# Kernel tuning notes

Hardware: AMD Instinct MI355X
Metric: run time of the kernel (lower is better)

The kernel has to match this reference:

```python
import jax, jax.numpy as jnp
import numpy as np

MARGIN = 0.05
TEMP = 14.0
LAM = 9.0      # opt.lambda_softmax
EPS = 1e-8
B, R, W, D, NCLS = 128, 36, 32, 256, 10


def setup_inputs() -> dict:
    key = jax.random.key(0)
    ks = jax.random.split(key, 7)
    im = jax.random.normal(ks[0], (B, R, D), jnp.float32)
    s = jax.random.normal(ks[1], (B, W, D), jnp.float32)
    s_l = jax.random.randint(ks[2], (B,), W // 2, W + 1)          # caption lengths in [16, 32]
    reg_l = jax.random.randint(ks[3], (B,), R // 2, R + 1)        # valid region counts
    im_mask = (jnp.arange(R)[None, :] < reg_l[:, None]).astype(jnp.float32)
    query_id = jax.random.randint(ks[4], (B,), 0, B)
    class_scores = jax.random.normal(ks[5], (B, NCLS), jnp.float32)
    class_labels = jax.random.randint(ks[6], (B,), 0, NCLS)
    return dict(im=im, s=s, s_l=s_l, im_mask=im_mask, query_id=query_id,
                class_scores=class_scores, class_labels=class_labels)


def _xattn_scores(im, s, s_l, im_mask):
    """Vectorized xattn_score_t2i. im:(B,R,D) images, s:(C,W,D) captions.
    Returns scores (n_image, n_caption). Zeroing pad words reproduces the
    original per-caption truncation (pad words contribute 0 to the word-dim
    l2 norm and are excluded from the final mean)."""
    wmask = (jnp.arange(W)[None, :] < s_l[:, None]).astype(s.dtype)   # (C,W)
    cap = s * wmask[:, :, None]                                        # (C,W,D)
    # attn[c,b,r,w] = <images[b,r], cap[c,w]>  (bmm in func_attention)
    attn = jnp.einsum('brd,cwd->cbrw', im, cap)
    attn = jax.nn.leaky_relu(attn, 0.1)
    # masked l2norm over the word dim (dim=2 in torch), mask over regions
    m = im_mask[None, :, :, None]                                      # (1,B,R,1)
    X = attn + (1.0 - m)
    nrm = jnp.sqrt(jnp.sum(X * X, axis=3, keepdims=True)) + EPS
    attn = (X / nrm) * m                                               # (C,B,R,W)
    # masked softmax over regions, per (caption, word); smooth = LAM
    x = jnp.swapaxes(attn, 2, 3) * LAM                                 # (C,B,W,R)
    mx = jnp.max(x, axis=3, keepdims=True)                             # unmasked max, as in source
    y = jnp.exp(x - mx) * im_mask[None, :, None, :]
    y = y / jnp.sum(y, axis=3, keepdims=True)
    # weightedContext[c,b,w,d] = sum_r images[b,r,d] * y[c,b,w,r]
    wctx = jnp.einsum('brd,cbwr->cbwd', im, y)
    # cosine similarity over d, then mean over the n_word valid words
    w12 = jnp.einsum('cwd,cbwd->cbw', cap, wctx)
    n1 = jnp.linalg.norm(cap, axis=2)                                  # (C,W)
    n2 = jnp.linalg.norm(wctx, axis=3)                                 # (C,B,W)
    cos = w12 / jnp.maximum(n1[:, None, :] * n2, EPS)
    row = jnp.sum(cos * wmask[:, None, :], axis=2) / s_l[:, None].astype(cos.dtype)
    return row.T                                                       # (n_image, n_caption)


def _contrastive_loss(im, s, s_l, im_mask, query_id):
    scores = _xattn_scores(im, s, s_l, im_mask)
    n = scores.shape[0]
    # label[i] = -100 (ignored) if query_id[i] appeared at some j < i, else i
    eq = query_id[:, None] == query_id[None, :]
    dup = jnp.any(jnp.tril(eq, k=-1), axis=1)
    labels = jnp.where(dup, -100, jnp.arange(n))
    logits = (scores - jnp.eye(n, dtype=scores.dtype) * MARGIN) * TEMP
    logZ = jax.nn.logsumexp(logits, axis=1)
    picked = jnp.take_along_axis(logits, jnp.maximum(labels, 0)[:, None], axis=1)[:, 0]
    valid = (labels >= 0).astype(scores.dtype)
    return jnp.sum((logZ - picked) * valid) / jnp.maximum(jnp.sum(valid), 1.0)


def reference(im, s, s_l, im_mask, query_id, class_scores, class_labels):
    # use_atten=True, use_label=False, use_mmd=False path of ContrastiveLoss
    return _contrastive_loss(im, s, s_l, im_mask, query_id)
```

## Files before the change

### kernel.cpp

```cpp
#include <hip/hip_runtime.h>
#include <hip/hip_bf16.h>
#include <math.h>

#define NB 128
#define NR 36
#define NW 32
#define ND 256

#define MARGINf 0.05f
#define TEMPf   14.0f
#define LAMf    9.0f
#define EPSf    1e-8f
#define LOG2Ef  1.4426950408889634f
#define INV_LOG2Ef 0.6931471805599453f

typedef _Float16 f16x8 __attribute__((ext_vector_type(8)));
typedef _Float16 f16x4 __attribute__((ext_vector_type(4)));
typedef float    f32x4 __attribute__((ext_vector_type(4)));

#define WS_SCORES 0
#define WS_N1     16384
#define WS_GW     20480
#define GW_H      3072
#define WS_IMW    217088
#define IMW_H     12288
#define WS_SHW    1003520
#define SHW_H     8192

__global__ __launch_bounds__(256) void prep5_kernel(
    const float* __restrict__ im, const float* __restrict__ s,
    const int* __restrict__ s_l, float* __restrict__ ws)
{
    const int t = threadIdx.x;
    const int bid = blockIdx.x;

    __shared__ __align__(16) float    s_imf[NR * 260];
    __shared__ __align__(16) _Float16 s_frag[24 * 512];
    __shared__ __align__(16) _Float16 s_G[48 * 72];

    if (bid < NB) {
        const int b = bid;
        const float4* im4 = (const float4*)(im + (size_t)b * NR * ND);
        for (int i = t; i < NR * 64; i += 256) {
            int r = i >> 6, c4 = i & 63;
            *(float4*)&s_imf[r * 260 + 4 * c4] = im4[i];
        }
        for (int i = t; i < 1728; i += 256) ((unsigned int*)s_G)[i] = 0u;
        __syncthreads();

        _Float16* imw = (_Float16*)(ws + WS_IMW) + (size_t)b * IMW_H;
        for (int i = t; i < 24 * 64; i += 256) {
            const int f = i >> 6, l = i & 63;
            const int mt = f >> 3, ks = f & 7;
            const int lmi = l & 15, kgi = l >> 4;
            const int r = mt * 16 + lmi;
            f16x8 h;
            if (r < NR) {
                const int k0 = ks * 32 + kgi * 8;
                const float4 a  = *(const float4*)&s_imf[r * 260 + k0];
                const float4 bb = *(const float4*)&s_imf[r * 260 + k0 + 4];
                h[0] = (_Float16)a.x;  h[1] = (_Float16)a.y;
                h[2] = (_Float16)a.z;  h[3] = (_Float16)a.w;
                h[4] = (_Float16)bb.x; h[5] = (_Float16)bb.y;
                h[6] = (_Float16)bb.z; h[7] = (_Float16)bb.w;
            } else {
#pragma unroll
                for (int k = 0; k < 8; ++k) h[k] = (_Float16)0.f;
            }
            *(f16x8*)(imw + f * 512 + l * 8) = h;
            *(f16x8*)(s_frag + f * 512 + l * 8) = h;
        }
        __syncthreads();

        {
            const int wv = t >> 6, lane = t & 63;
            const int lmi = lane & 15, kgi = lane >> 4;
            for (int p = wv; p < 9; p += 4) {
                const int ta = p / 3, tb = p - ta * 3;
                f32x4 acc = (f32x4){0.f, 0.f, 0.f, 0.f};
#pragma unroll
                for (int ks = 0; ks < 8; ++ks) {
                    f16x8 a  = *(const f16x8*)(s_frag + (ta * 8 + ks) * 512 + lane * 8);
                    f16x8 bb = *(const f16x8*)(s_frag + (tb * 8 + ks) * 512 + lane * 8);
                    acc = __builtin_amdgcn_mfma_f32_16x16x32_f16(a, bb, acc, 0, 0, 0);
                }
#pragma unroll
                for (int v = 0; v < 4; ++v) {
                    const int row = ta * 16 + kgi * 4 + v;
                    s_G[row * 72 + tb * 16 + lmi] = (_Float16)acc[v];
                }
            }
        }
        __syncthreads();

        _Float16* Gw = (_Float16*)(ws + WS_GW) + (size_t)b * GW_H;
        for (int i = t; i < 6 * 64; i += 256) {
            const int f = i >> 6, l = i & 63;
            const int rt = f >> 1, ks = f & 1;
            const int lmi = l & 15, kgi = l >> 4;
            f16x8 h = *(const f16x8*)&s_G[(rt * 16 + lmi) * 72 + ks * 32 + kgi * 8];
            *(f16x8*)((_Float16*)Gw + f * 512 + l * 8) = h;
        }
    } else {
        const int b = bid - NB;
        const int sl = s_l[b];
        _Float16* shw = (_Float16*)(ws + WS_SHW) + (size_t)b * SHW_H;
        const float4* s4 = (const float4*)(s + (size_t)b * NW * ND);

        for (int i = t; i < 16 * 64; i += 256) {
            const int f = i >> 6, l = i & 63;
            const int nt = f >> 3, ks = f & 7;
            const int lmi = l & 15, kgi = l >> 4;
            const int w = nt * 16 + lmi;
            f16x8 h;
            if (w < sl) {
                const int k0 = ks * 32 + kgi * 8;
                const float4 a  = s4[w * 64 + (k0 >> 2)];
                const float4 bb = s4[w * 64 + (k0 >> 2) + 1];
                h[0] = (_Float16)a.x;  h[1] = (_Float16)a.y;
                h[2] = (_Float16)a.z;  h[3] = (_Float16)a.w;
                h[4] = (_Float16)bb.x; h[5] = (_Float16)bb.y;
                h[6] = (_Float16)bb.z; h[7] = (_Float16)bb.w;
            } else {
#pragma unroll
                for (int k = 0; k < 8; ++k) h[k] = (_Float16)0.f;
            }
            *(f16x8*)(shw + f * 512 + l * 8) = h;
        }

        {
            const int w = t >> 3, g = t & 7;
            float acc = 0.f;
            for (int j = 0; j < 8; ++j) {
                float4 v = s4[w * 64 + g * 8 + j];
                acc += v.x * v.x + v.y * v.y + v.z * v.z + v.w * v.w;
            }
            acc += __shfl_down(acc, 4, 8);
            acc += __shfl_down(acc, 2, 8);
            acc += __shfl_down(acc, 1, 8);
            if (g == 0) ws[WS_N1 + b * NW + w] = sqrtf(acc);
        }
    }
}

__global__ __launch_bounds__(256, 4) void wavefused5_kernel(
    const int* __restrict__ s_l, const float* __restrict__ im_mask,
    float* __restrict__ ws)
{
    const int t = threadIdx.x;
    const int wv = t >> 6, lane = t & 63;
    const int lm = lane & 15, kg = lane >> 4;
    const int b = blockIdx.y;
    const int c = blockIdx.x * 4 + wv;

    __shared__ _Float16 sE[4][32 * 72];

    const _Float16* aB = (const _Float16*)(ws + WS_IMW) + (size_t)b * IMW_H + lane * 8;
    const _Float16* bB = (const _Float16*)(ws + WS_SHW) + (size_t)c * SHW_H + lane * 8;
    const _Float16* gB = (const _Float16*)(ws + WS_GW) + (size_t)b * GW_H + lane * 8;

    float n1v[2];
#pragma unroll
    for (int nt = 0; nt < 2; ++nt)
        n1v[nt] = ws[WS_N1 + c * NW + nt * 16 + lm];
    float mr[12];
#pragma unroll
    for (int mt = 0; mt < 3; ++mt)
#pragma unroll
        for (int v = 0; v < 4; ++v) {
            const int r = mt * 16 + kg * 4 + v;
            mr[mt * 4 + v] = (r < NR) ? im_mask[b * NR + r] : 0.f;
        }
    const int sl = s_l[c];

    f32x4 accv[6];
#pragma unroll
    for (int i = 0; i < 6; ++i) accv[i] = (f32x4){0.f, 0.f, 0.f, 0.f};

    f16x8 af[2][3], bf[2][2];
#pragma unroll
    for (int mt = 0; mt < 3; ++mt) af[0][mt] = *(const f16x8*)(aB + (mt * 8 + 0) * 512);
#pragma unroll
    for (int nt = 0; nt < 2; ++nt) bf[0][nt] = *(const f16x8*)(bB + (nt * 8 + 0) * 512);

#pragma unroll
    for (int ks = 0; ks < 8; ++ks) {
        const int cur = ks & 1, nxt = cur ^ 1;
        if (ks < 7) {
#pragma unroll
            for (int mt = 0; mt < 3; ++mt)
                af[nxt][mt] = *(const f16x8*)(aB + (mt * 8 + ks + 1) * 512);
#pragma unroll
            for (int nt = 0; nt < 2; ++nt)
                bf[nxt][nt] = *(const f16x8*)(bB + (nt * 8 + ks + 1) * 512);
        }
#pragma unroll
        for (int mt = 0; mt < 3; ++mt)
#pragma unroll
            for (int nt = 0; nt < 2; ++nt)
                accv[mt * 2 + nt] = __builtin_amdgcn_mfma_f32_16x16x32_f16(af[cur][mt], bf[cur][nt], accv[mt * 2 + nt], 0, 0, 0);
    }

    f32x4 er[6];
    float coef[12];
#pragma unroll
    for (int mt = 0; mt < 3; ++mt)
#pragma unroll
        for (int v = 0; v < 4; ++v) {
            const int idx = mt * 4 + v;
            const float one_m = 1.f - mr[idx];
            float p = 0.f;
#pragma unroll
            for (int nt = 0; nt < 2; ++nt) {
                const float raw = accv[mt * 2 + nt][v];
                const float X = fmaxf(raw, 0.1f * raw) + one_m;
                er[mt * 2 + nt][v] = X;
                p += X * X;
            }
            p += __shfl_xor(p, 1);
            p += __shfl_xor(p, 2);
            p += __shfl_xor(p, 4);
            p += __shfl_xor(p, 8);
            coef[idx] = (LAMf * LOG2Ef) *
                        __builtin_amdgcn_rcpf(__builtin_amdgcn_sqrtf(p) + EPSf);
        }

    _Float16* sEw = &sE[wv][0];
    float den[2] = {0.f, 0.f}, Wv[2] = {0.f, 0.f};
#pragma unroll
    for (int nt = 0; nt < 2; ++nt) {
        const int w = nt * 16 + lm;
#pragma unroll
        for (int mt = 0; mt < 3; ++mt) {
            f16x4 pk;
#pragma unroll
            for (int v = 0; v < 4; ++v) {
                const int idx = mt * 4 + v;
                const float raw = accv[mt * 2 + nt][v];
                const float X   = er[mt * 2 + nt][v];
                const float E = __builtin_amdgcn_exp2f(X * coef[idx]) * mr[idx];
                er[mt * 2 + nt][v] = E;
                den[nt] += E;
                Wv[nt] += E * raw;
                pk[v] = (_Float16)E;
            }
            *(f16x4*)&sEw[w * 72 + mt * 16 + kg * 4] = pk;
        }
        f16x4 z4; z4[0] = z4[1] = z4[2] = z4[3] = (_Float16)0.f;
        *(f16x4*)&sEw[w * 72 + 48 + kg * 4] = z4;
    }
#pragma unroll
    for (int nt = 0; nt < 2; ++nt) {
        den[nt] += __shfl_xor(den[nt], 16);
        den[nt] += __shfl_xor(den[nt], 32);
        Wv[nt]  += __shfl_xor(Wv[nt], 16);
        Wv[nt]  += __shfl_xor(Wv[nt], 32);
    }

#pragma unroll
    for (int i = 0; i < 6; ++i) accv[i] = (f32x4){0.f, 0.f, 0.f, 0.f};
#pragma unroll
    for (int ks = 0; ks < 2; ++ks) {
        f16x8 ef[2], gf[3];
#pragma unroll
        for (int wt = 0; wt < 2; ++wt)
            ef[wt] = *(const f16x8*)&sEw[(wt * 16 + lm) * 72 + ks * 32 + kg * 8];
#pragma unroll
        for (int rt = 0; rt < 3; ++rt)
            gf[rt] = *(const f16x8*)(gB + (rt * 2 + ks) * 512);
#pragma unroll
        for (int rt = 0; rt < 3; ++rt)
#pragma unroll
            for (int wt = 0; wt < 2; ++wt)
                accv[rt * 2 + wt] = __builtin_amdgcn_mfma_f32_16x16x32_f16(gf[rt], ef[wt], accv[rt * 2 + wt], 0, 0, 0);
    }
    float n2v[2];
#pragma unroll
    for (int nt = 0; nt < 2; ++nt) {
        float p2 = 0.f;
#pragma unroll
        for (int rt = 0; rt < 3; ++rt)
#pragma unroll
            for (int v = 0; v < 4; ++v)
                p2 += accv[rt * 2 + nt][v] * er[rt * 2 + nt][v];
        p2 += __shfl_xor(p2, 16);
        p2 += __shfl_xor(p2, 32);
        n2v[nt] = p2;
    }

    {
        float tot = 0.f;
#pragma unroll
        for (int nt = 0; nt < 2; ++nt) {
            const int w = nt * 16 + lm;
            const float n2 = fmaxf(n2v[nt], 0.f);
            const float denom = fmaxf(n1v[nt] * __builtin_amdgcn_sqrtf(n2), EPSf * den[nt]);
            const float cosv = Wv[nt] * __builtin_amdgcn_rcpf(denom);
            tot += (w < sl) ? cosv : 0.f;
        }
        tot += __shfl_xor(tot, 1);
        tot += __shfl_xor(tot, 2);
        tot += __shfl_xor(tot, 4);
        tot += __shfl_xor(tot, 8);
        if (lane == 0) ws[WS_SCORES + b * NB + c] = tot * __builtin_amdgcn_rcpf((float)sl);
    }
}

__global__ __launch_bounds__(128) void loss_kernel(
    const float* __restrict__ scores, const int* __restrict__ qid,
    float* __restrict__ out)
{
    __shared__ int   s_q[NB];
    __shared__ float s_pa[2];
    __shared__ float s_pv[2];
    const int i = threadIdx.x;
    const int wvi = i >> 6, lane = i & 63;
    s_q[i] = qid[i];
    __syncthreads();

    const int q = s_q[i];
    bool dup = false;
    for (int j = 0; j < i; ++j) dup = dup || (s_q[j] == q);

    const float* row = scores + i * NB;
    float mx = -1e30f;
    for (int j = 0; j < NB; ++j) {
        float l = (row[j] - ((j == i) ? MARGINf : 0.f)) * TEMPf;
        mx = fmaxf(mx, l);
    }
    float sum = 0.f;
    for (int j = 0; j < NB; ++j) {
        float l = (row[j] - ((j == i) ? MARGINf : 0.f)) * TEMPf;
        sum += __builtin_amdgcn_exp2f((l - mx) * LOG2Ef);
    }
    const float logZ = mx + __builtin_amdgcn_logf(sum) * INV_LOG2Ef;
    const float picked = (row[i] - MARGINf) * TEMPf;
    const float valid = dup ? 0.f : 1.f;
    float a = (logZ - picked) * valid;
    float v = valid;
    a += __shfl_xor(a, 1);  v += __shfl_xor(v, 1);
    a += __shfl_xor(a, 2);  v += __shfl_xor(v, 2);
    a += __shfl_xor(a, 4);  v += __shfl_xor(v, 4);
    a += __shfl_xor(a, 8);  v += __shfl_xor(v, 8);
    a += __shfl_xor(a, 16); v += __shfl_xor(v, 16);
    a += __shfl_xor(a, 32); v += __shfl_xor(v, 32);
    if (lane == 0) { s_pa[wvi] = a; s_pv[wvi] = v; }
    __syncthreads();
    if (i == 0)
        out[0] = (s_pa[0] + s_pa[1]) / fmaxf(s_pv[0] + s_pv[1], 1.f);
}

extern "C" void kernel_launch(void* const* d_in, const int* in_sizes, int n_in,
                              void* d_out, int out_size, void* d_ws, size_t ws_size,
                              hipStream_t stream) {
    const float* im      = (const float*)d_in[0];
    const float* s       = (const float*)d_in[1];
    const int*   s_l     = (const int*)d_in[2];
    const float* im_mask = (const float*)d_in[3];
    const int*   qid     = (const int*)d_in[4];

    float* ws  = (float*)d_ws;
    float* out = (float*)d_out;

    prep5_kernel<<<2 * NB, 256, 0, stream>>>(im, s, s_l, ws);
    wavefused5_kernel<<<dim3(32, NB), 256, 0, stream>>>(s_l, im_mask, ws);
    loss_kernel<<<1, 128, 0, stream>>>(ws + WS_SCORES, qid, out);
}
```

Before: 126.9 us.

## Stage per-image operands in LDS and process two captions per wave

```diff
diff --git a/kernel.cpp b/kernel.cpp
--- a/kernel.cpp
+++ b/kernel.cpp
@@ -143,7 +143,7 @@
     }
 }
 
-__global__ __launch_bounds__(256, 4) void wavefused5_kernel(
+__global__ __launch_bounds__(256, 3) void wavefused6_kernel(
     const int* __restrict__ s_l, const float* __restrict__ im_mask,
     float* __restrict__ ws)
 {
@@ -151,18 +151,22 @@
     const int wv = t >> 6, lane = t & 63;
     const int lm = lane & 15, kg = lane >> 4;
     const int b = blockIdx.y;
-    const int c = blockIdx.x * 4 + wv;
-
-    __shared__ _Float16 sE[4][32 * 72];
-
-    const _Float16* aB = (const _Float16*)(ws + WS_IMW) + (size_t)b * IMW_H + lane * 8;
-    const _Float16* bB = (const _Float16*)(ws + WS_SHW) + (size_t)c * SHW_H + lane * 8;
-    const _Float16* gB = (const _Float16*)(ws + WS_GW) + (size_t)b * GW_H + lane * 8;
-
-    float n1v[2];
-#pragma unroll
-    for (int nt = 0; nt < 2; ++nt)
-        n1v[nt] = ws[WS_N1 + c * NW + nt * 16 + lm];
+
+    __shared__ __align__(16) _Float16 s_ops[30 * 512];
+    __shared__ __align__(16) _Float16 sE[4][32 * 72];
+
+    {
+        const _Float16* srcA = (const _Float16*)(ws + WS_IMW) + (size_t)b * IMW_H;
+        const _Float16* srcG = (const _Float16*)(ws + WS_GW) + (size_t)b * GW_H;
+        for (int i = t; i < 30 * 64; i += 256) {
+            const int f = i >> 6, l = i & 63;
+            f16x8 h = (f < 24)
+                ? *(const f16x8*)(srcA + f * 512 + l * 8)
+                : *(const f16x8*)(srcG + (f - 24) * 512 + l * 8);
+            *(f16x8*)(s_ops + f * 512 + l * 8) = h;
+        }
+    }
+
     float mr[12];
 #pragma unroll
     for (int mt = 0; mt < 3; ++mt)
@@ -171,138 +175,151 @@
             const int r = mt * 16 + kg * 4 + v;
             mr[mt * 4 + v] = (r < NR) ? im_mask[b * NR + r] : 0.f;
         }
-    const int sl = s_l[c];
-
-    f32x4 accv[6];
-#pragma unroll
-    for (int i = 0; i < 6; ++i) accv[i] = (f32x4){0.f, 0.f, 0.f, 0.f};
-
-    f16x8 af[2][3], bf[2][2];
-#pragma unroll
-    for (int mt = 0; mt < 3; ++mt) af[0][mt] = *(const f16x8*)(aB + (mt * 8 + 0) * 512);
-#pragma unroll
-    for (int nt = 0; nt < 2; ++nt) bf[0][nt] = *(const f16x8*)(bB + (nt * 8 + 0) * 512);
-
-#pragma unroll
-    for (int ks = 0; ks < 8; ++ks) {
-        const int cur = ks & 1, nxt = cur ^ 1;
-        if (ks < 7) {
+
+    __syncthreads();
+
+    _Float16* sEw = &sE[wv][0];
+
+#pragma unroll 1
+    for (int ci = 0; ci < 2; ++ci) {
+        const int c = blockIdx.x * 8 + wv * 2 + ci;
+        const _Float16* bB = (const _Float16*)(ws + WS_SHW) + (size_t)c * SHW_H + lane * 8;
+
+        float n1v[2];
+#pragma unroll
+        for (int nt = 0; nt < 2; ++nt)
+            n1v[nt] = ws[WS_N1 + c * NW + nt * 16 + lm];
+        const int sl = s_l[c];
+
+        f32x4 accv[6];
+#pragma unroll
+        for (int i = 0; i < 6; ++i) accv[i] = (f32x4){0.f, 0.f, 0.f, 0.f};
+
+        f16x8 bf[2][2];
+#pragma unroll
+        for (int nt = 0; nt < 2; ++nt) bf[0][nt] = *(const f16x8*)(bB + (nt * 8 + 0) * 512);
+
+#pragma unroll
+        for (int ks = 0; ks < 8; ++ks) {
+            const int cur = ks & 1, nxt = cur ^ 1;
+            if (ks < 7) {
+#pragma unroll
+                for (int nt = 0; nt < 2; ++nt)
+                    bf[nxt][nt] = *(const f16x8*)(bB + (nt * 8 + ks + 1) * 512);
+            }
+            f16x8 af[3];
 #pragma unroll
             for (int mt = 0; mt < 3; ++mt)
-                af[nxt][mt] = *(const f16x8*)(aB + (mt * 8 + ks + 1) * 512);
-#pragma unroll
-            for (int nt = 0; nt < 2; ++nt)
-                bf[nxt][nt] = *(const f16x8*)(bB + (nt * 8 + ks + 1) * 512);
-        }
+                af[mt] = *(const f16x8*)(s_ops + (mt * 8 + ks) * 512 + lane * 8);
+#pragma unroll
+            for (int mt = 0; mt < 3; ++mt)
+#pragma unroll
+                for (int nt = 0; nt < 2; ++nt)
+                    accv[mt * 2 + nt] = __builtin_amdgcn_mfma_f32_16x16x32_f16(af[mt], bf[cur][nt], accv[mt * 2 + nt], 0, 0, 0);
+        }
+
+        f32x4 er[6];
+        float coef[12];
 #pragma unroll
         for (int mt = 0; mt < 3; ++mt)
-#pragma unroll
-            for (int nt = 0; nt < 2; ++nt)
-                accv[mt * 2 + nt] = __builtin_amdgcn_mfma_f32_16x16x32_f16(af[cur][mt], bf[cur][nt], accv[mt * 2 + nt], 0, 0, 0);
-    }
-
-    f32x4 er[6];
-    float coef[12];
-#pragma unroll
-    for (int mt = 0; mt < 3; ++mt)
-#pragma unroll
-        for (int v = 0; v < 4; ++v) {
-            const int idx = mt * 4 + v;
-            const float one_m = 1.f - mr[idx];
-            float p = 0.f;
-#pragma unroll
-            for (int nt = 0; nt < 2; ++nt) {
-                const float raw = accv[mt * 2 + nt][v];
-                const float X = fmaxf(raw, 0.1f * raw) + one_m;
-                er[mt * 2 + nt][v] = X;
-                p += X * X;
-            }
-            p += __shfl_xor(p, 1);
-            p += __shfl_xor(p, 2);
-            p += __shfl_xor(p, 4);
-            p += __shfl_xor(p, 8);
-            coef[idx] = (LAMf * LOG2Ef) *
-                        __builtin_amdgcn_rcpf(__builtin_amdgcn_sqrtf(p) + EPSf);
-        }
-
-    _Float16* sEw = &sE[wv][0];
-    float den[2] = {0.f, 0.f}, Wv[2] = {0.f, 0.f};
-#pragma unroll
-    for (int nt = 0; nt < 2; ++nt) {
-        const int w = nt * 16 + lm;
-#pragma unroll
-        for (int mt = 0; mt < 3; ++mt) {
-            f16x4 pk;
 #pragma unroll
             for (int v = 0; v < 4; ++v) {
                 const int idx = mt * 4 + v;
-                const float raw = accv[mt * 2 + nt][v];
-                const float X   = er[mt * 2 + nt][v];
-                const float E = __builtin_amdgcn_exp2f(X * coef[idx]) * mr[idx];
-                er[mt * 2 + nt][v] = E;
-                den[nt] += E;
-                Wv[nt] += E * raw;
-                pk[v] = (_Float16)E;
-            }
-            *(f16x4*)&sEw[w * 72 + mt * 16 + kg * 4] = pk;
-        }
-        f16x4 z4; z4[0] = z4[1] = z4[2] = z4[3] = (_Float16)0.f;
-        *(f16x4*)&sEw[w * 72 + 48 + kg * 4] = z4;
-    }
-#pragma unroll
-    for (int nt = 0; nt < 2; ++nt) {
-        den[nt] += __shfl_xor(den[nt], 16);
-        den[nt] += __shfl_xor(den[nt], 32);
-        Wv[nt]  += __shfl_xor(Wv[nt], 16);
-        Wv[nt]  += __shfl_xor(Wv[nt], 32);
-    }
-
-#pragma unroll
-    for (int i = 0; i < 6; ++i) accv[i] = (f32x4){0.f, 0.f, 0.f, 0.f};
-#pragma unroll
-    for (int ks = 0; ks < 2; ++ks) {
-        f16x8 ef[2], gf[3];
-#pragma unroll
-        for (int wt = 0; wt < 2; ++wt)
-            ef[wt] = *(const f16x8*)&sEw[(wt * 16 + lm) * 72 + ks * 32 + kg * 8];
-#pragma unroll
-        for (int rt = 0; rt < 3; ++rt)
-            gf[rt] = *(const f16x8*)(gB + (rt * 2 + ks) * 512);
-#pragma unroll
-        for (int rt = 0; rt < 3; ++rt)
-#pragma unroll
-            for (int wt = 0; wt < 2; ++wt)
-                accv[rt * 2 + wt] = __builtin_amdgcn_mfma_f32_16x16x32_f16(gf[rt], ef[wt], accv[rt * 2 + wt], 0, 0, 0);
-    }
-    float n2v[2];
-#pragma unroll
-    for (int nt = 0; nt < 2; ++nt) {
-        float p2 = 0.f;
-#pragma unroll
-        for (int rt = 0; rt < 3; ++rt)
-#pragma unroll
-            for (int v = 0; v < 4; ++v)
-                p2 += accv[rt * 2 + nt][v] * er[rt * 2 + nt][v];
-        p2 += __shfl_xor(p2, 16);
-        p2 += __shfl_xor(p2, 32);
-        n2v[nt] = p2;
-    }
-
-    {
-        float tot = 0.f;
+                const float one_m = 1.f - mr[idx];
+                float p = 0.f;
+#pragma unroll
+                for (int nt = 0; nt < 2; ++nt) {
+                    const float raw = accv[mt * 2 + nt][v];
+                    const float X = fmaxf(raw, 0.1f * raw) + one_m;
+                    er[mt * 2 + nt][v] = X;
+                    p += X * X;
+                }
+                p += __shfl_xor(p, 1);
+                p += __shfl_xor(p, 2);
+                p += __shfl_xor(p, 4);
+                p += __shfl_xor(p, 8);
+                coef[idx] = (LAMf * LOG2Ef) *
+                            __builtin_amdgcn_rcpf(__builtin_amdgcn_sqrtf(p) + EPSf);
+            }
+
+        float den[2] = {0.f, 0.f}, Wv[2] = {0.f, 0.f};
 #pragma unroll
         for (int nt = 0; nt < 2; ++nt) {
             const int w = nt * 16 + lm;
-            const float n2 = fmaxf(n2v[nt], 0.f);
-            const float denom = fmaxf(n1v[nt] * __builtin_amdgcn_sqrtf(n2), EPSf * den[nt]);
-            const float cosv = Wv[nt] * __builtin_amdgcn_rcpf(denom);
-            tot += (w < sl) ? cosv : 0.f;
-        }
-        tot += __shfl_xor(tot, 1);
-        tot += __shfl_xor(tot, 2);
-        tot += __shfl_xor(tot, 4);
-        tot += __shfl_xor(tot, 8);
-        if (lane == 0) ws[WS_SCORES + b * NB + c] = tot * __builtin_amdgcn_rcpf((float)sl);
+#pragma unroll
+            for (int mt = 0; mt < 3; ++mt) {
+                f16x4 pk;
+#pragma unroll
+                for (int v = 0; v < 4; ++v) {
+                    const int idx = mt * 4 + v;
+                    const float raw = accv[mt * 2 + nt][v];
+                    const float X   = er[mt * 2 + nt][v];
+                    const float E = __builtin_amdgcn_exp2f(X * coef[idx]) * mr[idx];
+                    er[mt * 2 + nt][v] = E;
+                    den[nt] += E;
+                    Wv[nt] += E * raw;
+                    pk[v] = (_Float16)E;
+                }
+                *(f16x4*)&sEw[w * 72 + mt * 16 + kg * 4] = pk;
+            }
+            f16x4 z4; z4[0] = z4[1] = z4[2] = z4[3] = (_Float16)0.f;
+            *(f16x4*)&sEw[w * 72 + 48 + kg * 4] = z4;
+        }
+#pragma unroll
+        for (int nt = 0; nt < 2; ++nt) {
+            den[nt] += __shfl_xor(den[nt], 16);
+            den[nt] += __shfl_xor(den[nt], 32);
+            Wv[nt]  += __shfl_xor(Wv[nt], 16);
+            Wv[nt]  += __shfl_xor(Wv[nt], 32);
+        }
+
+#pragma unroll
+        for (int i = 0; i < 6; ++i) accv[i] = (f32x4){0.f, 0.f, 0.f, 0.f};
+#pragma unroll
+        for (int ks = 0; ks < 2; ++ks) {
+            f16x8 ef[2], gf[3];
+#pragma unroll
+            for (int wt = 0; wt < 2; ++wt)
+                ef[wt] = *(const f16x8*)&sEw[(wt * 16 + lm) * 72 + ks * 32 + kg * 8];
+#pragma unroll
+            for (int rt = 0; rt < 3; ++rt)
+                gf[rt] = *(const f16x8*)(s_ops + (24 + rt * 2 + ks) * 512 + lane * 8);
+#pragma unroll
+            for (int rt = 0; rt < 3; ++rt)
+#pragma unroll
+                for (int wt = 0; wt < 2; ++wt)
+                    accv[rt * 2 + wt] = __builtin_amdgcn_mfma_f32_16x16x32_f16(gf[rt], ef[wt], accv[rt * 2 + wt], 0, 0, 0);
+        }
+        float n2v[2];
+#pragma unroll
+        for (int nt = 0; nt < 2; ++nt) {
+            float p2 = 0.f;
+#pragma unroll
+            for (int rt = 0; rt < 3; ++rt)
+#pragma unroll
+                for (int v = 0; v < 4; ++v)
+                    p2 += accv[rt * 2 + nt][v] * er[rt * 2 + nt][v];
+            p2 += __shfl_xor(p2, 16);
+            p2 += __shfl_xor(p2, 32);
+            n2v[nt] = p2;
+        }
+
+        {
+            float tot = 0.f;
+#pragma unroll
+            for (int nt = 0; nt < 2; ++nt) {
+                const int w = nt * 16 + lm;
+                const float n2 = fmaxf(n2v[nt], 0.f);
+                const float denom = fmaxf(n1v[nt] * __builtin_amdgcn_sqrtf(n2), EPSf * den[nt]);
+                const float cosv = Wv[nt] * __builtin_amdgcn_rcpf(denom);
+                tot += (w < sl) ? cosv : 0.f;
+            }
+            tot += __shfl_xor(tot, 1);
+            tot += __shfl_xor(tot, 2);
+            tot += __shfl_xor(tot, 4);
+            tot += __shfl_xor(tot, 8);
+            if (lane == 0) ws[WS_SCORES + b * NB + c] = tot * __builtin_amdgcn_rcpf((float)sl);
+        }
     }
 }
 
@@ -363,6 +380,6 @@
     float* out = (float*)d_out;
 
     prep5_kernel<<<2 * NB, 256, 0, stream>>>(im, s, s_l, ws);
-    wavefused5_kernel<<<dim3(32, NB), 256, 0, stream>>>(s_l, im_mask, ws);
+    wavefused6_kernel<<<dim3(16, NB), 256, 0, stream>>>(s_l, im_mask, ws);
     loss_kernel<<<1, 128, 0, stream>>>(ws + WS_SCORES, qid, out);
 }
```

Result: slower. 200.9 us (+58.2%).
